# Kernel tuning notes

Measured on AMD Instinct MI355X. Metric: run time of the kernel, lower is better.

The kernel has to match this reference:

```python
import jax, jax.numpy as jnp
import numpy as np

B, S, D = 4, 2048, 1024
H = 16
DK = D // H  # 64
THETA = 10000.0


def setup_inputs() -> dict:
    key = jax.random.key(0)
    ks = jax.random.split(key, 5)
    scale = 1.0 / np.sqrt(D)
    return {
        "x": jax.random.normal(ks[0], (B, S, D), dtype=jnp.float32),
        "wq": jax.random.normal(ks[1], (D, D), dtype=jnp.float32) * scale,
        "wk": jax.random.normal(ks[2], (D, D), dtype=jnp.float32) * scale,
        "wv": jax.random.normal(ks[3], (D, D), dtype=jnp.float32) * scale,
        "wo": jax.random.normal(ks[4], (D, D), dtype=jnp.float32) * scale,
    }


def _rope(x, cos2, sin2):
    # x: [B, H, S, DK]; cos2/sin2: [S, DK]
    x_even = x[..., 0::2]
    x_odd = x[..., 1::2]
    x_rot = jnp.stack([-x_odd, x_even], axis=-1).reshape(x.shape)
    return x * cos2 + x_rot * sin2


def reference(x, wq, wk, wv, wo):
    b, s, d = x.shape
    # QKV projections (weights are [out, in]; y = x @ W^T)
    q = jnp.einsum("bsd,od->bso", x, wq).reshape(b, s, H, DK).swapaxes(1, 2)
    k = jnp.einsum("bsd,od->bso", x, wk).reshape(b, s, H, DK).swapaxes(1, 2)
    v = jnp.einsum("bsd,od->bso", x, wv).reshape(b, s, H, DK).swapaxes(1, 2)

    # RoPE tables for positions [0, s)
    inv_freq = 1.0 / (THETA ** (jnp.arange(0, DK, 2, dtype=jnp.float32) / DK))
    angles = jnp.arange(s, dtype=jnp.float32)[:, None] * inv_freq[None, :]  # [s, DK/2]
    cos2 = jnp.repeat(jnp.cos(angles), 2, axis=-1).astype(x.dtype)  # [s, DK]
    sin2 = jnp.repeat(jnp.sin(angles), 2, axis=-1).astype(x.dtype)
    q = _rope(q, cos2, sin2)
    k = _rope(k, cos2, sin2)

    # Naive quadratic attention with causal mask (matches source sdpa)
    scores = jnp.einsum("bhqd,bhkd->bhqk", q, k) / (DK ** 0.5)
    causal = jnp.tril(jnp.ones((s, s), dtype=jnp.float32))
    scores = jnp.where(causal == 0.0, -jnp.inf, scores)
    probs = jax.nn.softmax(scores, axis=-1)
    attn = jnp.einsum("bhqk,bhkd->bhqd", probs, v)

    attn = attn.swapaxes(1, 2).reshape(b, s, d)
    return jnp.einsum("bsd,od->bso", attn, wo)
```

## Files before the change

kernel.cpp:

```cpp
#include <hip/hip_runtime.h>


typedef _Float16 f16;
typedef _Float16 f16x4 __attribute__((ext_vector_type(4)));
typedef _Float16 f16x8 __attribute__((ext_vector_type(8)));
typedef float    f32x4 __attribute__((ext_vector_type(4)));
typedef __fp16   h16x2 __attribute__((ext_vector_type(2)));

typedef __attribute__((address_space(1))) void gvoid_t;
typedef __attribute__((address_space(3))) void lvoid_t;

#define GLD16(g, l) __builtin_amdgcn_global_load_lds( \
    (gvoid_t*)(const void*)(g), (lvoid_t*)(l), 16, 0, 0)

#define VMCNT(n) asm volatile("s_waitcnt vmcnt(" #n ")" ::: "memory")

__device__ __forceinline__ void bar() {
    __builtin_amdgcn_sched_barrier(0);
    __builtin_amdgcn_s_barrier();
    __builtin_amdgcn_sched_barrier(0);
}

constexpr int BB = 4, SS = 2048, DD = 1024, HH = 16, DKK = 64;
constexpr int MM = BB * SS;

__global__ void cvt_kernel(const float4* __restrict__ in, f16x4* __restrict__ out, int n4) {
    int stride = gridDim.x * blockDim.x;
    for (int i = blockIdx.x * blockDim.x + threadIdx.x; i < n4; i += stride) {
        float4 v = in[i];
        f16x4 o;
        o[0] = (f16)v.x; o[1] = (f16)v.y; o[2] = (f16)v.z; o[3] = (f16)v.w;
        out[i] = o;
    }
}

__global__ void cvt4_kernel(const float4* __restrict__ a, const float4* __restrict__ b,
                            const float4* __restrict__ c, const float4* __restrict__ d,
                            f16x4* __restrict__ out, int n4per) {
    const float4* srcs[4] = {a, b, c, d};
    const float4* src = srcs[blockIdx.y];
    f16x4* dst = out + (size_t)blockIdx.y * n4per;
    int stride = gridDim.x * blockDim.x;
    for (int i = blockIdx.x * blockDim.x + threadIdx.x; i < n4per; i += stride) {
        float4 v = src[i];
        f16x4 o;
        o[0] = (f16)v.x; o[1] = (f16)v.y; o[2] = (f16)v.z; o[3] = (f16)v.w;
        dst[i] = o;
    }
}

__global__ void rope_tab_kernel(float* __restrict__ ctab, float* __restrict__ stab) {
    int idx = blockIdx.x * blockDim.x + threadIdx.x;
    if (idx >= SS * DKK) return;
    int s = idx >> 6, dk = idx & 63, i = dk >> 1;
    float inv = powf(10000.0f, -(float)(2 * i) / (float)DKK);
    float ang = (float)s * inv;
    ctab[idx] = cosf(ang);
    stab[idx] = sinf(ang);
}

__device__ __forceinline__ void gemm_core(
    const f16* __restrict__ A, const f16* __restrict__ Bm,
    f16* As, f16* Bs, f32x4 (&acc)[4][4], int bm, int bn)
{
    const int tid  = threadIdx.x;
    const int lane = tid & 63, wid = tid >> 6;
    const int lrow = lane & 15, lk = lane >> 4;
    const int wm = (wid >> 1) * 64, wn = (wid & 1) * 64;

    const int r_ = tid >> 3, c_ = tid & 7;

    auto STAGE = [&](int buf, int k0) {
#pragma unroll
        for (int j = 0; j < 4; ++j) {
            int r = j * 32 + r_;
            int cs = (c_ ^ (r & 7)) * 8;
            GLD16(A  + (size_t)(bm + r) * 1024 + k0 + cs, As + buf * 8192 + (j * 256 + wid * 64) * 8);
            GLD16(Bm + (size_t)(bn + r) * 1024 + k0 + cs, Bs + buf * 8192 + (j * 256 + wid * 64) * 8);
        }
    };

    auto COMPUTE = [&](int buf) {
        const f16* Ab = As + buf * 8192;
        const f16* Bb = Bs + buf * 8192;
#pragma unroll
        for (int kk = 0; kk < 2; ++kk) {
            f16x8 af[4], bf[4];
#pragma unroll
            for (int mi = 0; mi < 4; ++mi) {
                int row = wm + mi * 16 + lrow;
                af[mi] = *(const f16x8*)&Ab[row * 64 + ((kk * 4 + lk) ^ (row & 7)) * 8];
            }
#pragma unroll
            for (int ni = 0; ni < 4; ++ni) {
                int row = wn + ni * 16 + lrow;
                bf[ni] = *(const f16x8*)&Bb[row * 64 + ((kk * 4 + lk) ^ (row & 7)) * 8];
            }
#pragma unroll
            for (int mi = 0; mi < 4; ++mi)
#pragma unroll
                for (int ni = 0; ni < 4; ++ni)
                    acc[mi][ni] = __builtin_amdgcn_mfma_f32_16x16x32_f16(
                        af[mi], bf[ni], acc[mi][ni], 0, 0, 0);
        }
    };

    STAGE(0, 0);
    int cur = 0;
#pragma unroll 1
    for (int t = 0; t < 16; ++t) {
        if (t < 15) { STAGE(cur ^ 1, (t + 1) * 64); VMCNT(8); }
        else        { VMCNT(0); }
        bar();
        COMPUTE(cur);
        bar();
        cur ^= 1;
    }
}

__global__ __launch_bounds__(256) void qkv_gemm(
    const f16* __restrict__ xb, const f16* __restrict__ wqkv,
    f16* __restrict__ Qr, f16* __restrict__ Kr, f16* __restrict__ Vt,
    const float* __restrict__ ctab, const float* __restrict__ stab)
{
    __shared__ __align__(16) f16 As[2 * 128 * 64];
    __shared__ __align__(16) f16 Bs[2 * 128 * 64];
    const int i = blockIdx.x;
    const int xcol = i >> 6;
    const int yrow = (i & 7) * 8 + ((i >> 3) & 7);
    const int bm = yrow * 128, bn = xcol * 128;
    const int z = bn >> 10;
    const int bnw = bn & 1023;

    f32x4 acc[4][4] = {};
    gemm_core(xb, wqkv, As, Bs, acc, bm, bn);

    const int tid = threadIdx.x, lane = tid & 63, wid = tid >> 6;
    const int lrow = lane & 15, lk = lane >> 4;
    const int wm = (wid >> 1) * 64, wn = (wid & 1) * 64;

    if (z == 2) {
#pragma unroll
        for (int mi = 0; mi < 4; ++mi)
#pragma unroll
            for (int ni = 0; ni < 4; ++ni)
#pragma unroll
                for (int r = 0; r < 4; ++r) {
                    int row = bm + wm + mi * 16 + lk * 4 + r;
                    int col = bnw + wn + ni * 16 + lrow;
                    int b = row >> 11, s = row & 2047, h = col >> 6, dk = col & 63;
                    Vt[((size_t)(b * HH + h) * DKK + dk) * SS + s] = (f16)acc[mi][ni][r];
                }
    } else {
        f16* Out = (z == 0) ? Qr : Kr;
        const float scale = (z == 0) ? 0.125f * 1.44269504088896f : 1.0f;
#pragma unroll
        for (int mi = 0; mi < 4; ++mi)
#pragma unroll
            for (int ni = 0; ni < 4; ++ni)
#pragma unroll
                for (int r = 0; r < 4; ++r) {
                    int row = bm + wm + mi * 16 + lk * 4 + r;
                    int col = bnw + wn + ni * 16 + lrow;
                    int b = row >> 11, s = row & 2047, h = col >> 6, dk = col & 63;
                    float v = acc[mi][ni][r];
                    float partner = __shfl_xor(v, 1);
                    float cc = ctab[s * DKK + dk], ssn = stab[s * DKK + dk];
                    float rot = (col & 1) ? partner : -partner;
                    float o = (v * cc + rot * ssn) * scale;
                    Out[((size_t)(b * HH + h) * SS + s) * DKK + dk] = (f16)o;
                }
    }
}

__global__ __launch_bounds__(256, 4) void attn_kernel(
    const f16* __restrict__ Q, const f16* __restrict__ K, const f16* __restrict__ Vt,
    f16* __restrict__ attnB)
{
    __shared__ __align__(16) f16 Ks[2][64 * 64];
    __shared__ __align__(16) f16 Vs[2][64 * 64];
    __shared__ __align__(16) f16 Ps[4][16 * 64];

    const int tid = threadIdx.x, lane = tid & 63, wid = tid >> 6;
    const int lrow = lane & 15, lk = lane >> 4;
    const int bx = blockIdx.x;
    const int qt = 31 - (bx >> 6);
    const int bh = (bx & 7) * 8 + ((bx >> 3) & 7);
    const int b = bh >> 4, h = bh & 15;

    const f16* Qb = Q  + (size_t)bh * SS * DKK;
    const f16* Kb = K  + (size_t)bh * SS * DKK;
    const f16* Vb = Vt + (size_t)bh * DKK * SS;
    f16* PsW = &Ps[wid][0];

    const int qw = qt * 64 + wid * 16;
    const int nt = qt + 1;
    const int q  = qw + lrow;

    f16x8 qf[2];
#pragma unroll
    for (int kk = 0; kk < 2; ++kk)
        qf[kk] = *(const f16x8*)&Qb[(size_t)q * DKK + kk * 32 + lk * 8];

    f32x4 oacc[4] = {};
    float mst = -1e30f, lst = 0.0f;
    int cur = 0;

#pragma unroll
    for (int j = 0; j < 2; ++j) {
        int ci = j * 256 + tid;
        int r = ci >> 3, c = ci & 7;
        int cs = (c ^ (r & 7)) * 8;
        GLD16(Kb + (size_t)r * DKK + cs, &Ks[cur][(j * 256 + wid * 64) * 8]);
        GLD16(Vb + (size_t)r * SS  + cs, &Vs[cur][(j * 256 + wid * 64) * 8]);
    }

#pragma unroll 1
    for (int t = 0; t < nt; ++t) {
        const int kv0 = t * 64;
        if (t + 1 < nt) {
            const int kvn = kv0 + 64;
#pragma unroll
            for (int j = 0; j < 2; ++j) {
                int ci = j * 256 + tid;
                int r = ci >> 3, c = ci & 7;
                int cs = (c ^ (r & 7)) * 8;
                GLD16(Kb + (size_t)(kvn + r) * DKK + cs, &Ks[cur ^ 1][(j * 256 + wid * 64) * 8]);
                GLD16(Vb + (size_t)r * SS + kvn + cs,    &Vs[cur ^ 1][(j * 256 + wid * 64) * 8]);
            }
            VMCNT(4);
        } else {
            VMCNT(0);
        }
        bar();

        f32x4 sacc[4] = {};
#pragma unroll
        for (int kk = 0; kk < 2; ++kk)
#pragma unroll
            for (int ni = 0; ni < 4; ++ni) {
                int row = ni * 16 + lrow;
                f16x8 kf = *(const f16x8*)&Ks[cur][row * 64 + ((kk * 4 + lk) ^ (row & 7)) * 8];
                sacc[ni] = __builtin_amdgcn_mfma_f32_16x16x32_f16(
                    kf, qf[kk], sacc[ni], 0, 0, 0);
            }

        if (kv0 + 63 > q) {
#pragma unroll
            for (int ni = 0; ni < 4; ++ni)
#pragma unroll
                for (int r = 0; r < 4; ++r)
                    if (kv0 + ni * 16 + lk * 4 + r > q) sacc[ni][r] = -1e30f;
        }
        float m0 = -1e30f;
#pragma unroll
        for (int ni = 0; ni < 4; ++ni) {
            float a  = fmaxf(sacc[ni][0], sacc[ni][1]);
            float b2 = fmaxf(sacc[ni][2], sacc[ni][3]);
            m0 = fmaxf(m0, fmaxf(a, b2));
        }
        m0 = fmaxf(m0, __shfl_xor(m0, 16));
        m0 = fmaxf(m0, __shfl_xor(m0, 32));
        if (!__all(m0 - mst <= 11.5f)) {
            const float mnew  = fmaxf(mst, m0);
            const float alpha = exp2f(mst - mnew);
            mst = mnew;
            lst *= alpha;
#pragma unroll
            for (int no = 0; no < 4; ++no)
#pragma unroll
                for (int r = 0; r < 4; ++r)
                    oacc[no][r] *= alpha;
        }
        const float mref = mst;
        float rsum = 0.0f;
#pragma unroll
        for (int ni = 0; ni < 4; ++ni) {
            float p0 = exp2f(sacc[ni][0] - mref);
            float p1 = exp2f(sacc[ni][1] - mref);
            float p2 = exp2f(sacc[ni][2] - mref);
            float p3 = exp2f(sacc[ni][3] - mref);
            rsum += (p0 + p1) + (p2 + p3);
            h16x2 w0 = __builtin_amdgcn_cvt_pkrtz(p0, p1);
            h16x2 w1 = __builtin_amdgcn_cvt_pkrtz(p2, p3);
            f16x4 w;
            w[0] = (f16)w0[0]; w[1] = (f16)w0[1];
            w[2] = (f16)w1[0]; w[3] = (f16)w1[1];
            const int c = ni * 2 + (lk >> 1);
            *(f16x4*)&PsW[lrow * 64 + ((c ^ (lrow & 7)) * 8) + (lk & 1) * 4] = w;
        }
        rsum += __shfl_xor(rsum, 16);
        rsum += __shfl_xor(rsum, 32);
        lst += rsum;

        f16x8 pa[2];
#pragma unroll
        for (int kk = 0; kk < 2; ++kk)
            pa[kk] = *(const f16x8*)&PsW[lrow * 64 + ((kk * 4 + lk) ^ (lrow & 7)) * 8];
#pragma unroll
        for (int kk = 0; kk < 2; ++kk)
#pragma unroll
            for (int no = 0; no < 4; ++no) {
                int row = no * 16 + lrow;
                f16x8 vf = *(const f16x8*)&Vs[cur][row * 64 + ((kk * 4 + lk) ^ (row & 7)) * 8];
                oacc[no] = __builtin_amdgcn_mfma_f32_16x16x32_f16(
                    vf, pa[kk], oacc[no], 0, 0, 0);
            }

        bar();
        cur ^= 1;
    }

    {
        const float rl = 1.0f / lst;
#pragma unroll
        for (int no = 0; no < 4; ++no) {
            f16x4 w;
#pragma unroll
            for (int r = 0; r < 4; ++r) w[r] = (f16)(oacc[no][r] * rl);
            *(f16x4*)&attnB[((size_t)(b * SS) + q) * DD + h * DKK + no * 16 + lk * 4] = w;
        }
    }
}

__global__ __launch_bounds__(256) void out_gemm(
    const f16* __restrict__ attnB, const f16* __restrict__ wob, float* __restrict__ out)
{
    __shared__ __align__(16) f16 As[2 * 128 * 64];
    __shared__ __align__(16) f16 Bs[2 * 128 * 64];
    const int i = blockIdx.x;
    const int xcol = i >> 6;
    const int yrow = (i & 7) * 8 + ((i >> 3) & 7);
    const int bm = yrow * 128, bn = xcol * 128;
    f32x4 acc[4][4] = {};
    gemm_core(attnB, wob, As, Bs, acc, bm, bn);
    const int tid = threadIdx.x, lane = tid & 63, wid = tid >> 6;
    const int lrow = lane & 15, lk = lane >> 4;
    const int wm = (wid >> 1) * 64, wn = (wid & 1) * 64;
#pragma unroll
    for (int mi = 0; mi < 4; ++mi)
#pragma unroll
        for (int ni = 0; ni < 4; ++ni)
#pragma unroll
            for (int r = 0; r < 4; ++r) {
                int row = bm + wm + mi * 16 + lk * 4 + r;
                int col = bn + wn + ni * 16 + lrow;
                out[(size_t)row * 1024 + col] = acc[mi][ni][r];
            }
}

extern "C" void kernel_launch(void* const* d_in, const int* in_sizes, int n_in,
                              void* d_out, int out_size, void* d_ws, size_t ws_size,
                              hipStream_t stream) {
    const float* x  = (const float*)d_in[0];
    const float* wq = (const float*)d_in[1];
    const float* wk = (const float*)d_in[2];
    const float* wv = (const float*)d_in[3];
    const float* wo = (const float*)d_in[4];
    float* out = (float*)d_out;

    constexpr size_t NXB = (size_t)MM * DD;
    constexpr size_t NW  = (size_t)DD * DD;
    f16* xb  = (f16*)d_ws;
    f16* wqkv = xb + NXB;
    f16* wob  = wqkv + 3 * NW;
    f16* Qr  = wob + NW;
    f16* Kr  = Qr  + NXB;
    f16* Vt  = Kr  + NXB;
    float* ctab = (float*)(Vt + NXB);
    float* stab = ctab + SS * DKK;
    f16* attnB = xb;

    cvt_kernel<<<2048, 256, 0, stream>>>((const float4*)x, (f16x4*)xb, (int)(NXB / 4));
    cvt4_kernel<<<dim3(512, 4), 256, 0, stream>>>((const float4*)wq, (const float4*)wk,
                                                  (const float4*)wv, (const float4*)wo,
                                                  (f16x4*)wqkv, (int)(NW / 4));
    rope_tab_kernel<<<(SS * DKK + 255) / 256, 256, 0, stream>>>(ctab, stab);

    qkv_gemm<<<1536, 256, 0, stream>>>(xb, wqkv, Qr, Kr, Vt, ctab, stab);
    attn_kernel<<<2048, 256, 0, stream>>>(Qr, Kr, Vt, attnB);
    out_gemm<<<512, 256, 0, stream>>>(attnB, wob, out);
}
```

Before: 179.0 us.

## Fuse fp32-to-fp16 conversion of x into QKV GEMM A-tile loading

Drops the separate conversion kernel for x. The QKV GEMM now loads fp32 A tiles into registers, converts them to fp16, and writes them into a single LDS buffer, while B keeps async global-to-LDS double buffering. This removes a full read and write pass over the x tensor, at the cost of register staging, a single A buffer and double the global bytes per A tile. It also applies small attention softmax tweaks: v_max3 for the row max, and packed fdot2 for the row sum computed on the fp16-rounded probabilities.

```diff
diff --git a/kernel.cpp b/kernel.cpp
--- a/kernel.cpp
+++ b/kernel.cpp
@@ -14,6 +14,7 @@
     (gvoid_t*)(const void*)(g), (lvoid_t*)(l), 16, 0, 0)
 
 #define VMCNT(n) asm volatile("s_waitcnt vmcnt(" #n ")" ::: "memory")
+#define LGKM0()  asm volatile("s_waitcnt lgkmcnt(0)" ::: "memory")
 
 __device__ __forceinline__ void bar() {
     __builtin_amdgcn_sched_barrier(0);
@@ -21,18 +22,14 @@
     __builtin_amdgcn_sched_barrier(0);
 }
 
+__device__ __forceinline__ float max3f(float a, float b, float c) {
+    float d;
+    asm("v_max3_f32 %0, %1, %2, %3" : "=v"(d) : "v"(a), "v"(b), "v"(c));
+    return d;
+}
+
 constexpr int BB = 4, SS = 2048, DD = 1024, HH = 16, DKK = 64;
 constexpr int MM = BB * SS;
-
-__global__ void cvt_kernel(const float4* __restrict__ in, f16x4* __restrict__ out, int n4) {
-    int stride = gridDim.x * blockDim.x;
-    for (int i = blockIdx.x * blockDim.x + threadIdx.x; i < n4; i += stride) {
-        float4 v = in[i];
-        f16x4 o;
-        o[0] = (f16)v.x; o[1] = (f16)v.y; o[2] = (f16)v.z; o[3] = (f16)v.w;
-        out[i] = o;
-    }
-}
 
 __global__ void cvt4_kernel(const float4* __restrict__ a, const float4* __restrict__ b,
                             const float4* __restrict__ c, const float4* __restrict__ d,
@@ -67,7 +64,6 @@
     const int lane = tid & 63, wid = tid >> 6;
     const int lrow = lane & 15, lk = lane >> 4;
     const int wm = (wid >> 1) * 64, wn = (wid & 1) * 64;
-
     const int r_ = tid >> 3, c_ = tid & 7;
 
     auto STAGE = [&](int buf, int k0) {
@@ -118,12 +114,97 @@
     }
 }
 
+__device__ __forceinline__ void gemm_core_a32(
+    const float* __restrict__ A, const f16* __restrict__ Bm,
+    f16* As, f16* Bs, f32x4 (&acc)[4][4], int bm, int bn)
+{
+    const int tid  = threadIdx.x;
+    const int lane = tid & 63, wid = tid >> 6;
+    const int lrow = lane & 15, lk = lane >> 4;
+    const int wm = (wid >> 1) * 64, wn = (wid & 1) * 64;
+    const int r_ = tid >> 3, c_ = tid & 7;
+
+    float4 ar[4][2];
+
+    auto A_LOAD = [&](int k0) {
+#pragma unroll
+        for (int j = 0; j < 4; ++j) {
+            int r = j * 32 + r_;
+            int cs = (c_ ^ (r & 7)) * 8;
+            const float* src = A + (size_t)(bm + r) * 1024 + k0 + cs;
+            ar[j][0] = *(const float4*)src;
+            ar[j][1] = *(const float4*)(src + 4);
+        }
+    };
+
+    auto CVT_DSW = [&]() {
+#pragma unroll
+        for (int j = 0; j < 4; ++j) {
+            f16x8 o;
+            o[0] = (f16)ar[j][0].x; o[1] = (f16)ar[j][0].y;
+            o[2] = (f16)ar[j][0].z; o[3] = (f16)ar[j][0].w;
+            o[4] = (f16)ar[j][1].x; o[5] = (f16)ar[j][1].y;
+            o[6] = (f16)ar[j][1].z; o[7] = (f16)ar[j][1].w;
+            *(f16x8*)&As[(j * 256 + tid) * 8] = o;
+        }
+    };
+
+    auto STAGE_B = [&](int buf, int k0) {
+#pragma unroll
+        for (int j = 0; j < 4; ++j) {
+            int r = j * 32 + r_;
+            int cs = (c_ ^ (r & 7)) * 8;
+            GLD16(Bm + (size_t)(bn + r) * 1024 + k0 + cs, Bs + buf * 8192 + (j * 256 + wid * 64) * 8);
+        }
+    };
+
+    auto COMPUTE = [&](int buf) {
+        const f16* Bb = Bs + buf * 8192;
+#pragma unroll
+        for (int kk = 0; kk < 2; ++kk) {
+            f16x8 af[4], bf[4];
+#pragma unroll
+            for (int mi = 0; mi < 4; ++mi) {
+                int row = wm + mi * 16 + lrow;
+                af[mi] = *(const f16x8*)&As[row * 64 + ((kk * 4 + lk) ^ (row & 7)) * 8];
+            }
+#pragma unroll
+            for (int ni = 0; ni < 4; ++ni) {
+                int row = wn + ni * 16 + lrow;
+                bf[ni] = *(const f16x8*)&Bb[row * 64 + ((kk * 4 + lk) ^ (row & 7)) * 8];
+            }
+#pragma unroll
+            for (int mi = 0; mi < 4; ++mi)
+#pragma unroll
+                for (int ni = 0; ni < 4; ++ni)
+                    acc[mi][ni] = __builtin_amdgcn_mfma_f32_16x16x32_f16(
+                        af[mi], bf[ni], acc[mi][ni], 0, 0, 0);
+        }
+    };
+
+    A_LOAD(0);
+    STAGE_B(0, 0);
+    int cur = 0;
+#pragma unroll 1
+    for (int t = 0; t < 16; ++t) {
+        CVT_DSW();
+        if (t < 15) { STAGE_B(cur ^ 1, (t + 1) * 64); VMCNT(4); }
+        else        { VMCNT(0); }
+        LGKM0();
+        bar();
+        if (t < 15) A_LOAD((t + 1) * 64);
+        COMPUTE(cur);
+        bar();
+        cur ^= 1;
+    }
+}
+
 __global__ __launch_bounds__(256) void qkv_gemm(
-    const f16* __restrict__ xb, const f16* __restrict__ wqkv,
+    const float* __restrict__ xf, const f16* __restrict__ wqkv,
     f16* __restrict__ Qr, f16* __restrict__ Kr, f16* __restrict__ Vt,
     const float* __restrict__ ctab, const float* __restrict__ stab)
 {
-    __shared__ __align__(16) f16 As[2 * 128 * 64];
+    __shared__ __align__(16) f16 As[128 * 64];
     __shared__ __align__(16) f16 Bs[2 * 128 * 64];
     const int i = blockIdx.x;
     const int xcol = i >> 6;
@@ -133,7 +214,7 @@
     const int bnw = bn & 1023;
 
     f32x4 acc[4][4] = {};
-    gemm_core(xb, wqkv, As, Bs, acc, bm, bn);
+    gemm_core_a32(xf, wqkv, As, Bs, acc, bm, bn);
 
     const int tid = threadIdx.x, lane = tid & 63, wid = tid >> 6;
     const int lrow = lane & 15, lk = lane >> 4;
@@ -197,6 +278,8 @@
     const int nt = qt + 1;
     const int q  = qw + lrow;
 
+    const h16x2 kOne = {(__fp16)1.0f, (__fp16)1.0f};
+
     f16x8 qf[2];
 #pragma unroll
     for (int kk = 0; kk < 2; ++kk)
@@ -255,9 +338,8 @@
         float m0 = -1e30f;
 #pragma unroll
         for (int ni = 0; ni < 4; ++ni) {
-            float a  = fmaxf(sacc[ni][0], sacc[ni][1]);
-            float b2 = fmaxf(sacc[ni][2], sacc[ni][3]);
-            m0 = fmaxf(m0, fmaxf(a, b2));
+            m0 = max3f(sacc[ni][0], sacc[ni][1], m0);
+            m0 = max3f(sacc[ni][2], sacc[ni][3], m0);
         }
         m0 = fmaxf(m0, __shfl_xor(m0, 16));
         m0 = fmaxf(m0, __shfl_xor(m0, 32));
@@ -273,22 +355,29 @@
                     oacc[no][r] *= alpha;
         }
         const float mref = mst;
-        float rsum = 0.0f;
+        float rsa = 0.0f, rsb = 0.0f;
 #pragma unroll
         for (int ni = 0; ni < 4; ++ni) {
             float p0 = exp2f(sacc[ni][0] - mref);
             float p1 = exp2f(sacc[ni][1] - mref);
             float p2 = exp2f(sacc[ni][2] - mref);
             float p3 = exp2f(sacc[ni][3] - mref);
-            rsum += (p0 + p1) + (p2 + p3);
             h16x2 w0 = __builtin_amdgcn_cvt_pkrtz(p0, p1);
             h16x2 w1 = __builtin_amdgcn_cvt_pkrtz(p2, p3);
+#if __has_builtin(__builtin_amdgcn_fdot2)
+            rsa = __builtin_amdgcn_fdot2(w0, kOne, rsa, false);
+            rsb = __builtin_amdgcn_fdot2(w1, kOne, rsb, false);
+#else
+            rsa += p0 + p1;
+            rsb += p2 + p3;
+#endif
             f16x4 w;
             w[0] = (f16)w0[0]; w[1] = (f16)w0[1];
             w[2] = (f16)w1[0]; w[3] = (f16)w1[1];
             const int c = ni * 2 + (lk >> 1);
             *(f16x4*)&PsW[lrow * 64 + ((c ^ (lrow & 7)) * 8) + (lk & 1) * 4] = w;
         }
+        float rsum = rsa + rsb;
         rsum += __shfl_xor(rsum, 16);
         rsum += __shfl_xor(rsum, 32);
         lst += rsum;
@@ -361,23 +450,21 @@
 
     constexpr size_t NXB = (size_t)MM * DD;
     constexpr size_t NW  = (size_t)DD * DD;
-    f16* xb  = (f16*)d_ws;
-    f16* wqkv = xb + NXB;
-    f16* wob  = wqkv + 3 * NW;
+    f16* attnB = (f16*)d_ws;
+    f16* wqkv  = attnB + NXB;
+    f16* wob   = wqkv + 3 * NW;
     f16* Qr  = wob + NW;
     f16* Kr  = Qr  + NXB;
     f16* Vt  = Kr  + NXB;
     float* ctab = (float*)(Vt + NXB);
     float* stab = ctab + SS * DKK;
-    f16* attnB = xb;
-
-    cvt_kernel<<<2048, 256, 0, stream>>>((const float4*)x, (f16x4*)xb, (int)(NXB / 4));
+
     cvt4_kernel<<<dim3(512, 4), 256, 0, stream>>>((const float4*)wq, (const float4*)wk,
                                                   (const float4*)wv, (const float4*)wo,
                                                   (f16x4*)wqkv, (int)(NW / 4));
     rope_tab_kernel<<<(SS * DKK + 255) / 256, 256, 0, stream>>>(ctab, stab);
 
-    qkv_gemm<<<1536, 256, 0, stream>>>(xb, wqkv, Qr, Kr, Vt, ctab, stab);
+    qkv_gemm<<<1536, 256, 0, stream>>>(x, wqkv, Qr, Kr, Vt, ctab, stab);
     attn_kernel<<<2048, 256, 0, stream>>>(Qr, Kr, Vt, attnB);
     out_gemm<<<512, 256, 0, stream>>>(attnB, wob, out);
 }
```

Result: slower. 185.5 us (+3.6%).
